# Optimization experiments

Measured on AMD Instinct MI355X. Metric: run time of the kernel, lower is better.

## Reference

```python
import jax, jax.numpy as jnp
import numpy as np
from jax import lax


def ternarize(w):
    # TWN-style ternarization: threshold delta = 0.7*mean|w|, scale alpha =
    # mean |w| over surviving entries; straight-through in backward.
    aw = jnp.abs(w)
    delta = 0.7 * jnp.mean(aw)
    mask = (aw > delta).astype(w.dtype)
    alpha = jnp.sum(aw * mask) / jnp.maximum(jnp.sum(mask), 1.0)
    q = alpha * jnp.sign(w) * mask
    return w + lax.stop_gradient(q - w)


def conv2d(x, w, b):
    # x: [N,C,H,W], w: [O,I,kh,kw]
    y = lax.conv_general_dilated(x, w, window_strides=(1, 1), padding='VALID',
                                 dimension_numbers=('NCHW', 'OIHW', 'NCHW'))
    return y + b[None, :, None, None]


def maxpool2(x):
    return lax.reduce_window(x, -jnp.inf, lax.max,
                             window_dimensions=(1, 1, 2, 2),
                             window_strides=(1, 1, 2, 2), padding='VALID')


def setup_inputs() -> dict:
    key = jax.random.key(0)
    ks = jax.random.split(key, 11)
    n_classes = 10
    x = jax.random.normal(ks[0], (1024, 1, 32, 32), dtype=jnp.float32)
    # Kaiming-ish scaled params
    w1 = jax.random.normal(ks[1], (32, 1, 5, 5), jnp.float32) * (1.0 / np.sqrt(1 * 25))
    b1 = jnp.zeros((32,), jnp.float32)
    w2 = jax.random.normal(ks[2], (64, 32, 5, 5), jnp.float32) * (1.0 / np.sqrt(32 * 25))
    b2 = jnp.zeros((64,), jnp.float32)
    w3 = jax.random.normal(ks[3], (120, 64, 5, 5), jnp.float32) * (1.0 / np.sqrt(64 * 25))
    b3 = jnp.zeros((120,), jnp.float32)
    fw1 = jax.random.normal(ks[4], (84, 120), jnp.float32) * (1.0 / np.sqrt(120))
    fb1 = jnp.zeros((84,), jnp.float32)
    fw2 = jax.random.normal(ks[5], (n_classes, 84), jnp.float32) * (1.0 / np.sqrt(84))
    fb2 = jnp.zeros((n_classes,), jnp.float32)
    return {"x": x, "w1": w1, "b1": b1, "w2": w2, "b2": b2,
            "w3": w3, "b3": b3, "fw1": fw1, "fb1": fb1, "fw2": fw2, "fb2": fb2}


def reference(x, w1, b1, w2, b2, w3, b3, fw1, fb1, fw2, fb2):
    h = jnp.tanh(conv2d(x, ternarize(w1), b1))   # [N,32,28,28]
    h = maxpool2(h)                              # [N,32,14,14]
    h = jnp.tanh(conv2d(h, ternarize(w2), b2))   # [N,64,10,10]
    h = maxpool2(h)                              # [N,64,5,5]
    h = jnp.tanh(conv2d(h, ternarize(w3), b3))   # [N,120,1,1]
    h = h.reshape(h.shape[0], -1)                # [N,120]
    h = jnp.tanh(h @ ternarize(fw1).T + fb1)     # [N,84]
    logits = h @ ternarize(fw2).T + fb2          # [N,n_classes]
    probs = jax.nn.softmax(logits, axis=1)
    return (logits, probs)
```

## Files before the change

### kernel.cpp

```cpp
#include <hip/hip_runtime.h>
#include <hip/hip_bf16.h>
#include <math.h>


typedef __attribute__((ext_vector_type(8))) short bf16x8;
typedef __attribute__((ext_vector_type(4))) float f32x4;

static const size_t OFF_PB    = 0;
static const size_t OFF_Q1T   = 256;
static const size_t OFF_W2B   = 1056;
static const size_t OFF_W3B   = 26656;
static const size_t OFF_FW1T  = 129056;
static const size_t OFF_FW2T  = 139136;
static const size_t OFF_P2B   = 139976;
static const size_t OFF_H3    = 959176;

#define BPT 16

__device__ __forceinline__ ushort f2bf(float v) {
    unsigned u = __float_as_uint(v);
    unsigned r = (u + 0x7FFFu + ((u >> 16) & 1u)) >> 16;
    return (ushort)r;
}

__device__ __forceinline__ void tensor_select(int tensor,
        const float* w1, const float* w2, const float* w3,
        const float* fw1, const float* fw2,
        const float*& src, int& O, int& K) {
    switch (tensor) {
        case 0: src = w1;  O = 32;  K = 25;   break;
        case 1: src = w2;  O = 64;  K = 800;  break;
        case 2: src = w3;  O = 120; K = 1600; break;
        case 3: src = fw1; O = 84;  K = 120;  break;
        default: src = fw2; O = 10; K = 84;   break;
    }
}

__device__ __forceinline__ float block_sum_256(float v, float* sbuf) {
    #pragma unroll
    for (int off = 32; off > 0; off >>= 1) v += __shfl_down(v, off);
    const int wid = threadIdx.x >> 6;
    if ((threadIdx.x & 63) == 0) sbuf[wid] = v;
    __syncthreads();
    return sbuf[0] + sbuf[1] + sbuf[2] + sbuf[3];
}

__device__ __forceinline__ float alpha_of(const float* pb, int tensor) {
    float s1 = 0.f, c = 0.f;
    #pragma unroll
    for (int i = 0; i < BPT; ++i) {
        s1 += pb[80 + tensor * BPT + i];
        c  += pb[160 + tensor * BPT + i];
    }
    return s1 / fmaxf(c, 1.0f);
}

__global__ __launch_bounds__(256)
void tern_pass1(const float* w1, const float* w2, const float* w3,
                const float* fw1, const float* fw2, float* pb) {
    __shared__ float sbuf[4];
    const int tensor = blockIdx.x / BPT;
    const int blk    = blockIdx.x % BPT;
    const float* src; int O, K;
    tensor_select(tensor, w1, w2, w3, fw1, fw2, src, O, K);
    const int n = O * K;
    float s = 0.f;
    for (int i = blk * 256 + threadIdx.x; i < n; i += BPT * 256)
        s += fabsf(src[i]);
    s = block_sum_256(s, sbuf);
    if (threadIdx.x == 0) pb[tensor * BPT + blk] = s;
}

__global__ __launch_bounds__(256)
void tern_pass2(const float* w1, const float* w2, const float* w3,
                const float* fw1, const float* fw2,
                float* q1t, ushort* w2b, ushort* w3b,
                float* fw1t, float* fw2t, float* pb) {
    __shared__ float sbuf[4];
    const int tensor = blockIdx.x / BPT;
    const int blk    = blockIdx.x % BPT;
    const float* src; int O, K;
    tensor_select(tensor, w1, w2, w3, fw1, fw2, src, O, K);
    const int n = O * K;
    float tot = 0.f;
    #pragma unroll
    for (int i = 0; i < BPT; ++i) tot += pb[tensor * BPT + i];
    const float delta = 0.7f * tot / (float)n;

    const ushort BP = 0x3F80u, BN = 0xBF80u;
    float s1 = 0.f, cnt = 0.f;

    if (tensor == 2) {
        for (int i = blk * 256 + threadIdx.x; i < 128 * 1600; i += BPT * 256) {
            ushort qb = 0;
            if (i < n) {
                float w = src[i];
                float aw = fabsf(w);
                if (aw > delta) { s1 += aw; cnt += 1.f; qb = (w > 0.f) ? BP : BN; }
            }
            w3b[i] = qb;
        }
    } else if (tensor == 1) {
        for (int i = blk * 256 + threadIdx.x; i < n; i += BPT * 256) {
            float w = src[i];
            float aw = fabsf(w);
            ushort qb = 0;
            if (aw > delta) { s1 += aw; cnt += 1.f; qb = (w > 0.f) ? BP : BN; }
            int oc = i / 800;
            int r  = i - oc * 800;
            int ic = r / 25;
            int tap = r - ic * 25;
            w2b[oc * 800 + tap * 32 + ic] = qb;
        }
    } else {
        float* dst = (tensor == 0) ? q1t : (tensor == 3) ? fw1t : fw2t;
        for (int i = blk * 256 + threadIdx.x; i < n; i += BPT * 256) {
            float w = src[i];
            float aw = fabsf(w);
            float q = 0.f;
            if (aw > delta) { s1 += aw; cnt += 1.f; q = (w > 0.f) ? 1.f : -1.f; }
            int o = i / K;
            int k = i - o * K;
            dst[k * O + o] = q;
        }
    }
    s1 = block_sum_256(s1, sbuf);
    __syncthreads();
    cnt = block_sum_256(cnt, sbuf);
    if (threadIdx.x == 0) {
        pb[80 + tensor * BPT + blk]  = s1;
        pb[160 + tensor * BPT + blk] = cnt;
    }
}

template<int TBASE, int TCNT>
__device__ __forceinline__ void conv2_phase(
        const ushort* __restrict__ w2b, const ushort* sxt,
        int n0, int mt0, int lane, f32x4 acc[4][2]) {
    const int col = lane & 15, quad = lane >> 4;
    bf16x8 bfr[TCNT][2];
    #pragma unroll
    for (int i = 0; i < TCNT; ++i) {
        const int tap = TBASE + i;
        #pragma unroll
        for (int np = 0; np < 2; ++np) {
            const int oc = n0 + np * 16 + col;
            bfr[i][np] = *(const bf16x8*)(w2b + (oc * 25 + tap) * 32 + quad * 8);
        }
    }
    #pragma unroll
    for (int mi = 0; mi < 4; ++mi) {
        int m = (mt0 + mi) * 16 + col;
        m = m < 100 ? m : 99;
        const int oh = m / 10, ow = m - oh * 10;
        const ushort* abase = sxt + (oh * 14 + ow) * 40 + quad * 8;
        #pragma unroll
        for (int i = 0; i < TCNT; ++i) {
            const int tap = TBASE + i;
            const int kh = tap / 5, kw = tap - kh * 5;
            bf16x8 af = *(const bf16x8*)(abase + (kh * 14 + kw) * 40);
            acc[mi][0] = __builtin_amdgcn_mfma_f32_16x16x32_bf16(af, bfr[i][0], acc[mi][0], 0, 0, 0);
            acc[mi][1] = __builtin_amdgcn_mfma_f32_16x16x32_bf16(af, bfr[i][1], acc[mi][1], 0, 0, 0);
        }
    }
}

__global__ __launch_bounds__(256)
void conv12_kernel(const float* __restrict__ x, const float* __restrict__ q1t,
                   const float* __restrict__ b1, const ushort* __restrict__ w2b,
                   const float* __restrict__ b2, const float* __restrict__ pb,
                   ushort* __restrict__ p2b) {
    __shared__ __align__(16) ushort sxt[196 * 40];
    __shared__ float cbuf[64 * 100];
    __shared__ float salpha[2];
    float* sx = cbuf;
    float* sw = cbuf + 1024;

    const int n = blockIdx.x;
    const int t = threadIdx.x;
    {
        const float4* src = (const float4*)(x + (size_t)n * 1024);
        if (t < 256) ((float4*)sx)[t] = src[t];
        if (t < 200) ((float4*)sw)[t] = ((const float4*)q1t)[t];
        if (t == 0) salpha[0] = alpha_of(pb, 0);
        if (t == 1) salpha[1] = alpha_of(pb, 1);
    }
    __syncthreads();

    const float a1 = salpha[0];
    const int ocg  = t >> 5;
    const int pos0 = t & 31;
    float bias[4];
    #pragma unroll
    for (int o = 0; o < 4; ++o) bias[o] = b1[ocg * 4 + o];

    for (int pos = pos0; pos < 196; pos += 32) {
        const int ph = pos / 14, pw = pos - ph * 14;
        const int r0 = 2 * ph, c0 = 2 * pw;
        float acc[4][4] = {};
        const float4* wp = (const float4*)sw + ocg;
        #pragma unroll
        for (int kh = 0; kh < 5; ++kh) {
            const float* xr = sx + (r0 + kh) * 32 + c0;
            #pragma unroll
            for (int kw = 0; kw < 5; ++kw) {
                const float4 w4 = *wp; wp += 8;
                const float x00 = xr[kw],      x01 = xr[kw + 1];
                const float x10 = xr[kw + 32], x11 = xr[kw + 33];
                acc[0][0] = fmaf(w4.x, x00, acc[0][0]);
                acc[0][1] = fmaf(w4.x, x01, acc[0][1]);
                acc[0][2] = fmaf(w4.x, x10, acc[0][2]);
                acc[0][3] = fmaf(w4.x, x11, acc[0][3]);
                acc[1][0] = fmaf(w4.y, x00, acc[1][0]);
                acc[1][1] = fmaf(w4.y, x01, acc[1][1]);
                acc[1][2] = fmaf(w4.y, x10, acc[1][2]);
                acc[1][3] = fmaf(w4.y, x11, acc[1][3]);
                acc[2][0] = fmaf(w4.z, x00, acc[2][0]);
                acc[2][1] = fmaf(w4.z, x01, acc[2][1]);
                acc[2][2] = fmaf(w4.z, x10, acc[2][2]);
                acc[2][3] = fmaf(w4.z, x11, acc[2][3]);
                acc[3][0] = fmaf(w4.w, x00, acc[3][0]);
                acc[3][1] = fmaf(w4.w, x01, acc[3][1]);
                acc[3][2] = fmaf(w4.w, x10, acc[3][2]);
                acc[3][3] = fmaf(w4.w, x11, acc[3][3]);
            }
        }
        ushort4 qv;
        {
            float m0 = fmaxf(fmaxf(acc[0][0], acc[0][1]), fmaxf(acc[0][2], acc[0][3]));
            float m1 = fmaxf(fmaxf(acc[1][0], acc[1][1]), fmaxf(acc[1][2], acc[1][3]));
            float m2 = fmaxf(fmaxf(acc[2][0], acc[2][1]), fmaxf(acc[2][2], acc[2][3]));
            float m3 = fmaxf(fmaxf(acc[3][0], acc[3][1]), fmaxf(acc[3][2], acc[3][3]));
            qv.x = f2bf(tanhf(fmaf(a1, m0, bias[0])));
            qv.y = f2bf(tanhf(fmaf(a1, m1, bias[1])));
            qv.z = f2bf(tanhf(fmaf(a1, m2, bias[2])));
            qv.w = f2bf(tanhf(fmaf(a1, m3, bias[3])));
        }
        *(ushort4*)(&sxt[pos * 40 + ocg * 4]) = qv;
    }
    __syncthreads();

    const int wave = t >> 6, lane = t & 63;
    const int n0  = (wave & 1) * 32;
    const int mt0 = (wave >> 1) * 4;
    f32x4 acc2[4][2] = {};
    conv2_phase<0, 13>(w2b, sxt, n0, mt0, lane, acc2);
    conv2_phase<13, 12>(w2b, sxt, n0, mt0, lane, acc2);

    {
        const int col = lane & 15, quad = lane >> 4;
        #pragma unroll
        for (int mi = 0; mi < 4; ++mi) {
            const int mrow = (mt0 + mi) * 16 + quad * 4;
            if (mrow < 100) {
                #pragma unroll
                for (int np = 0; np < 2; ++np) {
                    const int oc = n0 + np * 16 + col;
                    *(f32x4*)(&cbuf[oc * 100 + mrow]) = acc2[mi][np];
                }
            }
        }
    }
    __syncthreads();

    const float a2 = salpha[1];
    for (int idx = t; idx < 1600; idx += 256) {
        const int oc = idx / 25, r = idx - oc * 25;
        const int ph = r / 5, pw = r - ph * 5;
        const float* c0 = &cbuf[oc * 100 + ph * 20 + pw * 2];
        float m = fmaxf(fmaxf(c0[0], c0[1]), fmaxf(c0[10], c0[11]));
        p2b[(size_t)n * 1600 + idx] = f2bf(tanhf(fmaf(a2, m, b2[oc])));
    }
}

template<int STEPS>
__device__ __forceinline__ void conv3_chunk(const ushort* Abase, const ushort* B0,
                                            const ushort* B1, f32x4& acc0, f32x4& acc1) {
    #pragma unroll
    for (int s = 0; s < STEPS; ++s) {
        bf16x8 af = *(const bf16x8*)(Abase + s * 32);
        bf16x8 b0 = *(const bf16x8*)(B0 + s * 32);
        bf16x8 b1 = *(const bf16x8*)(B1 + s * 32);
        acc0 = __builtin_amdgcn_mfma_f32_16x16x32_bf16(af, b0, acc0, 0, 0, 0);
        acc1 = __builtin_amdgcn_mfma_f32_16x16x32_bf16(af, b1, acc1, 0, 0, 0);
    }
}

__global__ __launch_bounds__(256)
void conv3_mfma(const ushort* __restrict__ p2b, const ushort* __restrict__ w3b,
                const float* __restrict__ b3, const float* __restrict__ pb,
                float* __restrict__ h3) {
    __shared__ float red[4][64][8];
    __shared__ float salpha;
    const int t = threadIdx.x;
    const int wave = t >> 6, lane = t & 63;
    const int mt = blockIdx.x >> 2;
    const int npair = blockIdx.x & 3;
    const int col = lane & 15, quad = lane >> 4;
    const int kstart = (wave < 2) ? wave * 13 : 26 + (wave - 2) * 12;

    if (t == 0) salpha = alpha_of(pb, 2);

    const ushort* Abase = p2b + (size_t)(mt * 16 + col) * 1600 + kstart * 32 + quad * 8;
    const ushort* B0 = w3b + (size_t)(npair * 32 + col) * 1600 + kstart * 32 + quad * 8;
    const ushort* B1 = B0 + 16 * 1600;

    f32x4 acc0 = {}, acc1 = {};
    if (wave < 2) conv3_chunk<13>(Abase, B0, B1, acc0, acc1);
    else          conv3_chunk<12>(Abase, B0, B1, acc0, acc1);

    #pragma unroll
    for (int r = 0; r < 4; ++r) {
        red[wave][lane][r]     = acc0[r];
        red[wave][lane][4 + r] = acc1[r];
    }
    __syncthreads();

    {
        const float a3 = salpha;
        const int l = t & 63, vh = t >> 6;
        const int lcol = l & 15, lquad = l >> 4;
        const int img = mt * 16 + lquad * 4 + vh;
        #pragma unroll
        for (int j = 0; j < 2; ++j) {
            const int v = j * 4 + vh;
            float s = red[0][l][v] + red[1][l][v] + red[2][l][v] + red[3][l][v];
            const int oc = npair * 32 + j * 16 + lcol;
            if (oc < 120) h3[(size_t)img * 120 + oc] = tanhf(fmaf(a3, s, b3[oc]));
        }
    }
}

__global__ __launch_bounds__(128)
void fc_kernel(const float* __restrict__ h3, const float* __restrict__ fw1t,
               const float* __restrict__ fb1, const float* __restrict__ fw2t,
               const float* __restrict__ fb2, const float* __restrict__ pb,
               float* __restrict__ out) {
    const int n = blockIdx.x;
    __shared__ float sh[120];
    __shared__ float sh4[84];
    __shared__ float sl[10];
    __shared__ float salpha[2];
    const int t = threadIdx.x;
    if (t < 120) sh[t] = h3[(size_t)n * 120 + t];
    if (t == 120) salpha[0] = alpha_of(pb, 3);
    if (t == 121) salpha[1] = alpha_of(pb, 4);
    __syncthreads();
    if (t < 84) {
        const float af1 = salpha[0];
        float a = 0.f;
        #pragma unroll 4
        for (int k = 0; k < 120; ++k) a = fmaf(fw1t[k * 84 + t], sh[k], a);
        sh4[t] = tanhf(fmaf(af1, a, fb1[t]));
    }
    __syncthreads();
    if (t < 10) {
        const float af2 = salpha[1];
        float a = 0.f;
        #pragma unroll 4
        for (int k = 0; k < 84; ++k) a = fmaf(fw2t[k * 10 + t], sh4[k], a);
        const float lg = fmaf(af2, a, fb2[t]);
        sl[t] = lg;
        out[(size_t)n * 10 + t] = lg;
    }
    __syncthreads();
    if (t < 10) {
        float m = -INFINITY;
        #pragma unroll
        for (int i = 0; i < 10; ++i) m = fmaxf(m, sl[i]);
        float s = 0.f;
        #pragma unroll
        for (int i = 0; i < 10; ++i) s += expf(sl[i] - m);
        out[10240 + (size_t)n * 10 + t] = expf(sl[t] - m) / s;
    }
}

extern "C" void kernel_launch(void* const* d_in, const int* in_sizes, int n_in,
                              void* d_out, int out_size, void* d_ws, size_t ws_size,
                              hipStream_t stream) {
    const float* x   = (const float*)d_in[0];
    const float* w1  = (const float*)d_in[1];
    const float* b1  = (const float*)d_in[2];
    const float* w2  = (const float*)d_in[3];
    const float* b2  = (const float*)d_in[4];
    const float* w3  = (const float*)d_in[5];
    const float* b3  = (const float*)d_in[6];
    const float* fw1 = (const float*)d_in[7];
    const float* fb1 = (const float*)d_in[8];
    const float* fw2 = (const float*)d_in[9];
    const float* fb2 = (const float*)d_in[10];

    float* ws = (float*)d_ws;
    float*  pb   = ws + OFF_PB;
    float*  q1t  = ws + OFF_Q1T;
    ushort* w2b  = (ushort*)(ws + OFF_W2B);
    ushort* w3b  = (ushort*)(ws + OFF_W3B);
    float*  fw1t = ws + OFF_FW1T;
    float*  fw2t = ws + OFF_FW2T;
    ushort* p2b  = (ushort*)(ws + OFF_P2B);
    float*  h3   = ws + OFF_H3;
    float*  out  = (float*)d_out;

    tern_pass1<<<5 * BPT, 256, 0, stream>>>(w1, w2, w3, fw1, fw2, pb);
    tern_pass2<<<5 * BPT, 256, 0, stream>>>(w1, w2, w3, fw1, fw2,
                                            q1t, w2b, w3b, fw1t, fw2t, pb);
    conv12_kernel<<<1024, 256, 0, stream>>>(x, q1t, b1, w2b, b2, pb, p2b);
    conv3_mfma<<<256, 256, 0, stream>>>(p2b, w3b, b3, pb, h3);
    fc_kernel<<<1024, 128, 0, stream>>>(h3, fw1t, fb1, fw2t, fb2, pb, out);
}
```

Measured before the change: 166.1 us.

## Use fast exp-based tanh, pre-reduce pooling in registers, vectorize conv1 input loads

Replaces tanhf with an __expf-based tanh approximation in all epilogues. Horizontal max-pooling of conv2 outputs is done in registers before the LDS store, which halves the staging buffer and cuts LDS traffic and footprint, possibly improving occupancy. Conv1 input rows are loaded once per kh as float2 vectors instead of per-tap scalar LDS reads. The fast tanh slightly changes numerics, especially near zero.

Result: no change. 163.2 us (-1.8%).

```diff
diff --git a/kernel.cpp b/kernel.cpp
--- a/kernel.cpp
+++ b/kernel.cpp
@@ -21,6 +21,12 @@
     unsigned u = __float_as_uint(v);
     unsigned r = (u + 0x7FFFu + ((u >> 16) & 1u)) >> 16;
     return (ushort)r;
+}
+
+__device__ __forceinline__ float tanh_fast(float x) {
+    float e = __expf(-2.0f * fabsf(x));
+    float r = 1.0f - 2.0f * e / (1.0f + e);
+    return copysignf(r, x);
 }
 
 __device__ __forceinline__ void tensor_select(int tensor,
@@ -171,10 +177,10 @@
                    const float* __restrict__ b2, const float* __restrict__ pb,
                    ushort* __restrict__ p2b) {
     __shared__ __align__(16) ushort sxt[196 * 40];
-    __shared__ float cbuf[64 * 100];
+    __shared__ __align__(16) float hbuf[64 * 50];
     __shared__ float salpha[2];
-    float* sx = cbuf;
-    float* sw = cbuf + 1024;
+    float* sx = hbuf;
+    float* sw = hbuf + 1024;
 
     const int n = blockIdx.x;
     const int t = threadIdx.x;
@@ -202,11 +208,19 @@
         #pragma unroll
         for (int kh = 0; kh < 5; ++kh) {
             const float* xr = sx + (r0 + kh) * 32 + c0;
+            float2 pa0 = *(const float2*)&xr[0];
+            float2 pa1 = *(const float2*)&xr[2];
+            float2 pa2 = *(const float2*)&xr[4];
+            float2 pb0 = *(const float2*)&xr[32];
+            float2 pb1 = *(const float2*)&xr[34];
+            float2 pb2 = *(const float2*)&xr[36];
+            const float xa[6] = {pa0.x, pa0.y, pa1.x, pa1.y, pa2.x, pa2.y};
+            const float xb[6] = {pb0.x, pb0.y, pb1.x, pb1.y, pb2.x, pb2.y};
             #pragma unroll
             for (int kw = 0; kw < 5; ++kw) {
                 const float4 w4 = *wp; wp += 8;
-                const float x00 = xr[kw],      x01 = xr[kw + 1];
-                const float x10 = xr[kw + 32], x11 = xr[kw + 33];
+                const float x00 = xa[kw], x01 = xa[kw + 1];
+                const float x10 = xb[kw], x11 = xb[kw + 1];
                 acc[0][0] = fmaf(w4.x, x00, acc[0][0]);
                 acc[0][1] = fmaf(w4.x, x01, acc[0][1]);
                 acc[0][2] = fmaf(w4.x, x10, acc[0][2]);
@@ -231,10 +245,10 @@
             float m1 = fmaxf(fmaxf(acc[1][0], acc[1][1]), fmaxf(acc[1][2], acc[1][3]));
             float m2 = fmaxf(fmaxf(acc[2][0], acc[2][1]), fmaxf(acc[2][2], acc[2][3]));
             float m3 = fmaxf(fmaxf(acc[3][0], acc[3][1]), fmaxf(acc[3][2], acc[3][3]));
-            qv.x = f2bf(tanhf(fmaf(a1, m0, bias[0])));
-            qv.y = f2bf(tanhf(fmaf(a1, m1, bias[1])));
-            qv.z = f2bf(tanhf(fmaf(a1, m2, bias[2])));
-            qv.w = f2bf(tanhf(fmaf(a1, m3, bias[3])));
+            qv.x = f2bf(tanh_fast(fmaf(a1, m0, bias[0])));
+            qv.y = f2bf(tanh_fast(fmaf(a1, m1, bias[1])));
+            qv.z = f2bf(tanh_fast(fmaf(a1, m2, bias[2])));
+            qv.w = f2bf(tanh_fast(fmaf(a1, m3, bias[3])));
         }
         *(ushort4*)(&sxt[pos * 40 + ocg * 4]) = qv;
     }
@@ -256,7 +270,10 @@
                 #pragma unroll
                 for (int np = 0; np < 2; ++np) {
                     const int oc = n0 + np * 16 + col;
-                    *(f32x4*)(&cbuf[oc * 100 + mrow]) = acc2[mi][np];
+                    float2 hm;
+                    hm.x = fmaxf(acc2[mi][np][0], acc2[mi][np][1]);
+                    hm.y = fmaxf(acc2[mi][np][2], acc2[mi][np][3]);
+                    *(float2*)(&hbuf[oc * 50 + (mrow >> 1)]) = hm;
                 }
             }
         }
@@ -267,9 +284,9 @@
     for (int idx = t; idx < 1600; idx += 256) {
         const int oc = idx / 25, r = idx - oc * 25;
         const int ph = r / 5, pw = r - ph * 5;
-        const float* c0 = &cbuf[oc * 100 + ph * 20 + pw * 2];
-        float m = fmaxf(fmaxf(c0[0], c0[1]), fmaxf(c0[10], c0[11]));
-        p2b[(size_t)n * 1600 + idx] = f2bf(tanhf(fmaf(a2, m, b2[oc])));
+        const float* hb = &hbuf[oc * 50 + ph * 10 + pw];
+        float m = fmaxf(hb[0], hb[5]);
+        p2b[(size_t)n * 1600 + idx] = f2bf(tanh_fast(fmaf(a2, m, b2[oc])));
     }
 }
 
@@ -326,7 +343,7 @@
             const int v = j * 4 + vh;
             float s = red[0][l][v] + red[1][l][v] + red[2][l][v] + red[3][l][v];
             const int oc = npair * 32 + j * 16 + lcol;
-            if (oc < 120) h3[(size_t)img * 120 + oc] = tanhf(fmaf(a3, s, b3[oc]));
+            if (oc < 120) h3[(size_t)img * 120 + oc] = tanh_fast(fmaf(a3, s, b3[oc]));
         }
     }
 }
@@ -351,7 +368,7 @@
         float a = 0.f;
         #pragma unroll 4
         for (int k = 0; k < 120; ++k) a = fmaf(fw1t[k * 84 + t], sh[k], a);
-        sh4[t] = tanhf(fmaf(af1, a, fb1[t]));
+        sh4[t] = tanh_fast(fmaf(af1, a, fb1[t]));
     }
     __syncthreads();
     if (t < 10) {
```
